# Kernel optimization log

Measured on AMD Instinct MI355X. Metric: run time of the kernel, lower is better.

## Reference

```python
import jax, jax.numpy as jnp
import numpy as np

B, S, C, T = 16, 64, 20, 2048
_DIMS = [(20, 20), (20, 20), (20, 20), (20, 10), (10, 1)]


def setup_inputs() -> dict:
    key = jax.random.key(0)
    keys = jax.random.split(key, 1 + 2 * len(_DIMS))
    inp = {"data": jax.random.normal(keys[0], (B, S, C, T), dtype=jnp.float32)}
    for i, (din, dout) in enumerate(_DIMS):
        # weights stored (in, out); scaled like torch's default Linear init
        inp[f"W{i+1}"] = jax.random.normal(keys[1 + 2 * i], (din, dout), dtype=jnp.float32) / jnp.sqrt(jnp.float32(din))
        inp[f"b{i+1}"] = jax.random.normal(keys[2 + 2 * i], (dout,), dtype=jnp.float32) * 0.05
    return inp


def _mlp(x, Ws, bs):
    # x: (..., in_dim); five Linear+ReLU layers, final ReLU included
    h = x
    for W, b in zip(Ws, bs):
        h = jax.nn.relu(h @ W + b)
    return h


def reference(data, W1, b1, W2, b2, W3, b3, W4, b4, W5, b5):
    # data: (B, S, C, T) -> per-time-point features (B, S, T, C)
    x = jnp.swapaxes(data, 2, 3)
    y = _mlp(x, (W1, W2, W3, W4, W5), (b1, b2, b3, b4, b5))[..., 0]  # (B, S, T)
    t = y.shape[-1]
    yc = y - y.mean(axis=-1, keepdims=True)
    cov = jnp.einsum('bst,but->bsu', yc, yc) / jnp.float32(t - 1)  # (B, S, S)
    d = jnp.sqrt(jnp.diagonal(cov, axis1=1, axis2=2))  # (B, S)
    corr = cov / (d[:, :, None] * d[:, None, :])
    corr = jnp.clip(corr, -1.0, 1.0)  # torch.corrcoef clips real output
    return 1.0 - corr
```

## Files before the change

kernel.cpp:

```cpp
#include <hip/hip_runtime.h>

#define Bn 16
#define Sn 64
#define Cn 20
#define Tn 2048
#define TPB 256

template <int NJ>
__device__ __forceinline__ void layer2(const float (&in)[2][20], float (&out)[2][20],
                                       const float* __restrict__ WT,
                                       const float* __restrict__ bb) {
    #pragma unroll
    for (int j = 0; j < NJ; ++j) {
        float a0 = bb[j], a1 = bb[j];
        const float4* wr = (const float4*)(WT + j * 20);
        #pragma unroll
        for (int q = 0; q < 5; ++q) {
            const float4 w = wr[q];
            a0 = fmaf(in[0][4 * q + 0], w.x, a0);  a1 = fmaf(in[1][4 * q + 0], w.x, a1);
            a0 = fmaf(in[0][4 * q + 1], w.y, a0);  a1 = fmaf(in[1][4 * q + 1], w.y, a1);
            a0 = fmaf(in[0][4 * q + 2], w.z, a0);  a1 = fmaf(in[1][4 * q + 2], w.z, a1);
            a0 = fmaf(in[0][4 * q + 3], w.w, a0);  a1 = fmaf(in[1][4 * q + 3], w.w, a1);
        }
        out[0][j] = fmaxf(a0, 0.f);
        out[1][j] = fmaxf(a1, 0.f);
    }
}

__global__ __launch_bounds__(256) void mlp_kernel(
    const float* __restrict__ data,
    const float* __restrict__ W1, const float* __restrict__ b1,
    const float* __restrict__ W2, const float* __restrict__ b2,
    const float* __restrict__ W3, const float* __restrict__ b3,
    const float* __restrict__ W4, const float* __restrict__ b4,
    const float* __restrict__ W5, const float* __restrict__ b5,
    float* __restrict__ y, double* __restrict__ Rp)
{
    __shared__ __align__(16) float sW1T[400], sW2T[400], sW3T[400], sW4T[200];
    __shared__ float sW5[10], sb1[20], sb2[20], sb3[20], sb4[10], sb5v[1];
    __shared__ double rbuf[TPB];

    const int tid = threadIdx.x;
    for (int i = tid; i < 400; i += TPB) {
        const int j = i / 20, c = i % 20;
        sW1T[i] = W1[c * 20 + j];
        sW2T[i] = W2[c * 20 + j];
        sW3T[i] = W3[c * 20 + j];
    }
    if (tid < 200) { const int j = tid / 20, c = tid % 20; sW4T[tid] = W4[c * 10 + j]; }
    if (tid < 20) { sb1[tid] = b1[tid]; sb2[tid] = b2[tid]; sb3[tid] = b3[tid]; }
    if (tid < 10) { sW5[tid] = W5[tid]; sb4[tid] = b4[tid]; }
    if (tid == 0) sb5v[0] = b5[0];
    __syncthreads();

    const int bs = blockIdx.x >> 2;
    const int qt = blockIdx.x & 3;
    const float* base = data + (size_t)bs * Cn * Tn;
    const int t0 = qt * (Tn / 4) + tid * 2;

    float x[2][20], h[2][20];
    #pragma unroll
    for (int c = 0; c < 20; ++c) {
        const float2 v = *(const float2*)&base[c * Tn + t0];
        x[0][c] = v.x; x[1][c] = v.y;
    }

    layer2<20>(x, h, sW1T, sb1);
    layer2<20>(h, x, sW2T, sb2);
    layer2<20>(x, h, sW3T, sb3);
    layer2<10>(h, x, sW4T, sb4);

    float yv[2];
    #pragma unroll
    for (int m = 0; m < 2; ++m) {
        float yy = sb5v[0];
        #pragma unroll
        for (int i = 0; i < 10; ++i) yy = fmaf(x[m][i], sW5[i], yy);
        yv[m] = fmaxf(yy, 0.f);
    }
    float2 st; st.x = yv[0]; st.y = yv[1];
    *(float2*)&y[(size_t)bs * Tn + t0] = st;

    rbuf[tid] = (double)yv[0] + (double)yv[1];
    __syncthreads();
    for (int off = 128; off > 0; off >>= 1) {
        if (tid < off) rbuf[tid] += rbuf[tid + off];
        __syncthreads();
    }
    if (tid == 0) Rp[blockIdx.x] = rbuf[0];
}

__global__ __launch_bounds__(256) void cov_kernel(
    const float* __restrict__ y, const double* __restrict__ Rp,
    double* __restrict__ covd)
{
    __shared__ __align__(16) float ysc[Tn];
    __shared__ double rbuf[TPB];

    const int tid = threadIdx.x;
    const int lane = tid & 63, wv = tid >> 6;
    const int ut = blockIdx.x & 3;
    const int bs = blockIdx.x >> 2;
    const int b = bs >> 6;

    const double ms = (Rp[bs * 4] + Rp[bs * 4 + 1] + Rp[bs * 4 + 2] + Rp[bs * 4 + 3]) * (1.0 / Tn);
    const float* yrow = y + (size_t)bs * Tn;

    double lsum = 0.0;
    for (int t = tid; t < Tn; t += TPB) {
        const float v = (float)((double)yrow[t] - ms);
        ysc[t] = v;
        lsum += (double)v;
    }
    rbuf[tid] = lsum;
    __syncthreads();
    for (int off = 128; off > 0; off >>= 1) {
        if (tid < off) rbuf[tid] += rbuf[tid + off];
        __syncthreads();
    }
    const double sumYsc = rbuf[0];

    const float* ybase = y + (size_t)(b << 6) * Tn;
    const double* Rb = Rp + (b << 6) * 4;
    double* crow = covd + (size_t)bs * Sn;

    #pragma unroll
    for (int uu = 0; uu < 4; ++uu) {
        const int u = ut * 16 + wv * 4 + uu;
        const float* yu = ybase + (size_t)u * Tn;
        float acc = 0.f;
        #pragma unroll
        for (int k = 0; k < Tn / 256; ++k) {
            const int t = (k * 64 + lane) * 4;
            const float4 a = *(const float4*)&ysc[t];
            const float4 g = *(const float4*)&yu[t];
            acc = fmaf(a.x, g.x, acc);
            acc = fmaf(a.y, g.y, acc);
            acc = fmaf(a.z, g.z, acc);
            acc = fmaf(a.w, g.w, acc);
        }
        #pragma unroll
        for (int off = 32; off; off >>= 1) acc += __shfl_down(acc, off, 64);
        if (lane == 0) {
            const double mu = (Rb[u * 4] + Rb[u * 4 + 1] + Rb[u * 4 + 2] + Rb[u * 4 + 3]) * (1.0 / Tn);
            crow[u] = ((double)acc - mu * sumYsc) * (1.0 / (Tn - 1));
        }
    }
}

__global__ __launch_bounds__(256) void corr_kernel(
    const double* __restrict__ covd, float* __restrict__ out)
{
    const int i = blockIdx.x * TPB + threadIdx.x;
    if (i >= Bn * Sn * Sn) return;
    const int b = i / (Sn * Sn);
    const int rem = i % (Sn * Sn);
    const int s = rem / Sn, u = rem % Sn;
    const double css = covd[((size_t)b * Sn + s) * Sn + s];
    const double cuu = covd[((size_t)b * Sn + u) * Sn + u];
    const double csu = covd[i];
    double r = csu / sqrt(css * cuu);
    r = (r < -1.0) ? -1.0 : ((r > 1.0) ? 1.0 : r);
    out[i] = (float)(1.0 - r);
}

extern "C" void kernel_launch(void* const* d_in, const int* in_sizes, int n_in,
                              void* d_out, int out_size, void* d_ws, size_t ws_size,
                              hipStream_t stream) {
    const float* data = (const float*)d_in[0];
    const float* W1 = (const float*)d_in[1];  const float* b1 = (const float*)d_in[2];
    const float* W2 = (const float*)d_in[3];  const float* b2 = (const float*)d_in[4];
    const float* W3 = (const float*)d_in[5];  const float* b3 = (const float*)d_in[6];
    const float* W4 = (const float*)d_in[7];  const float* b4 = (const float*)d_in[8];
    const float* W5 = (const float*)d_in[9];  const float* b5 = (const float*)d_in[10];
    float* out = (float*)d_out;

    float* y = (float*)d_ws;
    double* covd = (double*)((char*)d_ws + (size_t)Bn * Sn * Tn * sizeof(float));
    double* Rp = covd + (size_t)Bn * Sn * Sn;

    mlp_kernel<<<Bn * Sn * 4, TPB, 0, stream>>>(data, W1, b1, W2, b2, W3, b3, W4, b4, W5, b5, y, Rp);
    cov_kernel<<<Bn * Sn * 4, TPB, 0, stream>>>(y, Rp, covd);
    corr_kernel<<<(Bn * Sn * Sn + TPB - 1) / TPB, TPB, 0, stream>>>(covd, out);
}
```

Measured before the change: 316.2 us.

## Rewrite covariance as split-K register-tiled SYRK in shared memory with atomics

```diff
diff --git a/kernel.cpp b/kernel.cpp
--- a/kernel.cpp
+++ b/kernel.cpp
@@ -5,6 +5,9 @@
 #define Cn 20
 #define Tn 2048
 #define TPB 256
+#define KS 8
+#define Kc (Tn / KS)
+#define PITCH 260
 
 template <int NJ>
 __device__ __forceinline__ void layer2(const float (&in)[2][20], float (&out)[2][20],
@@ -92,73 +95,83 @@
 
 __global__ __launch_bounds__(256) void cov_kernel(
     const float* __restrict__ y, const double* __restrict__ Rp,
-    double* __restrict__ covd)
+    float* __restrict__ covf)
 {
-    __shared__ __align__(16) float ysc[Tn];
-    __shared__ double rbuf[TPB];
+    __shared__ __align__(16) float S[64 * PITCH];
+    __shared__ double smean[64];
 
     const int tid = threadIdx.x;
-    const int lane = tid & 63, wv = tid >> 6;
-    const int ut = blockIdx.x & 3;
-    const int bs = blockIdx.x >> 2;
-    const int b = bs >> 6;
+    const int b  = blockIdx.x >> 3;
+    const int ks = blockIdx.x & 7;
 
-    const double ms = (Rp[bs * 4] + Rp[bs * 4 + 1] + Rp[bs * 4 + 2] + Rp[bs * 4 + 3]) * (1.0 / Tn);
-    const float* yrow = y + (size_t)bs * Tn;
+    if (tid < 64) {
+        const int q = ((b << 6) + tid) * 4;
+        smean[tid] = (Rp[q] + Rp[q + 1] + Rp[q + 2] + Rp[q + 3]) * (1.0 / Tn);
+    }
+    __syncthreads();
 
-    double lsum = 0.0;
-    for (int t = tid; t < Tn; t += TPB) {
-        const float v = (float)((double)yrow[t] - ms);
-        ysc[t] = v;
-        lsum += (double)v;
+    const float* ybase = y + (size_t)(b << 6) * Tn + ks * Kc;
+    #pragma unroll
+    for (int it = 0; it < (64 * Kc / 4) / TPB; ++it) {
+        const int f4 = tid + it * TPB;
+        const int row = f4 >> 6;
+        const int k4 = f4 & 63;
+        const float4 v = *(const float4*)&ybase[(size_t)row * Tn + k4 * 4];
+        const double m = smean[row];
+        float4 c;
+        c.x = (float)((double)v.x - m);
+        c.y = (float)((double)v.y - m);
+        c.z = (float)((double)v.z - m);
+        c.w = (float)((double)v.w - m);
+        *(float4*)&S[row * PITCH + k4 * 4] = c;
     }
-    rbuf[tid] = lsum;
     __syncthreads();
-    for (int off = 128; off > 0; off >>= 1) {
-        if (tid < off) rbuf[tid] += rbuf[tid + off];
-        __syncthreads();
+
+    const int ty = tid >> 4, tx = tid & 15;
+    float acc[4][4];
+    #pragma unroll
+    for (int a = 0; a < 4; ++a)
+        #pragma unroll
+        for (int j = 0; j < 4; ++j) acc[a][j] = 0.f;
+
+    for (int kq = 0; kq < Kc / 4; ++kq) {
+        float4 av[4], bv[4];
+        #pragma unroll
+        for (int a = 0; a < 4; ++a) av[a] = *(const float4*)&S[(ty + 16 * a) * PITCH + kq * 4];
+        #pragma unroll
+        for (int j = 0; j < 4; ++j) bv[j] = *(const float4*)&S[(tx + 16 * j) * PITCH + kq * 4];
+        #pragma unroll
+        for (int a = 0; a < 4; ++a)
+            #pragma unroll
+            for (int j = 0; j < 4; ++j) {
+                acc[a][j] = fmaf(av[a].x, bv[j].x, acc[a][j]);
+                acc[a][j] = fmaf(av[a].y, bv[j].y, acc[a][j]);
+                acc[a][j] = fmaf(av[a].z, bv[j].z, acc[a][j]);
+                acc[a][j] = fmaf(av[a].w, bv[j].w, acc[a][j]);
+            }
     }
-    const double sumYsc = rbuf[0];
 
-    const float* ybase = y + (size_t)(b << 6) * Tn;
-    const double* Rb = Rp + (b << 6) * 4;
-    double* crow = covd + (size_t)bs * Sn;
-
+    float* cb = covf + ((size_t)b << 12);
     #pragma unroll
-    for (int uu = 0; uu < 4; ++uu) {
-        const int u = ut * 16 + wv * 4 + uu;
-        const float* yu = ybase + (size_t)u * Tn;
-        float acc = 0.f;
+    for (int a = 0; a < 4; ++a) {
+        const int row = ty + 16 * a;
         #pragma unroll
-        for (int k = 0; k < Tn / 256; ++k) {
-            const int t = (k * 64 + lane) * 4;
-            const float4 a = *(const float4*)&ysc[t];
-            const float4 g = *(const float4*)&yu[t];
-            acc = fmaf(a.x, g.x, acc);
-            acc = fmaf(a.y, g.y, acc);
-            acc = fmaf(a.z, g.z, acc);
-            acc = fmaf(a.w, g.w, acc);
-        }
-        #pragma unroll
-        for (int off = 32; off; off >>= 1) acc += __shfl_down(acc, off, 64);
-        if (lane == 0) {
-            const double mu = (Rb[u * 4] + Rb[u * 4 + 1] + Rb[u * 4 + 2] + Rb[u * 4 + 3]) * (1.0 / Tn);
-            crow[u] = ((double)acc - mu * sumYsc) * (1.0 / (Tn - 1));
-        }
+        for (int j = 0; j < 4; ++j)
+            atomicAdd(&cb[(row << 6) + tx + 16 * j], acc[a][j]);
     }
 }
 
 __global__ __launch_bounds__(256) void corr_kernel(
-    const double* __restrict__ covd, float* __restrict__ out)
+    const float* __restrict__ covf, float* __restrict__ out)
 {
     const int i = blockIdx.x * TPB + threadIdx.x;
     if (i >= Bn * Sn * Sn) return;
     const int b = i / (Sn * Sn);
     const int rem = i % (Sn * Sn);
     const int s = rem / Sn, u = rem % Sn;
-    const double css = covd[((size_t)b * Sn + s) * Sn + s];
-    const double cuu = covd[((size_t)b * Sn + u) * Sn + u];
-    const double csu = covd[i];
+    const double css = (double)covf[((size_t)b * Sn + s) * Sn + s];
+    const double cuu = (double)covf[((size_t)b * Sn + u) * Sn + u];
+    const double csu = (double)covf[i];
     double r = csu / sqrt(css * cuu);
     r = (r < -1.0) ? -1.0 : ((r > 1.0) ? 1.0 : r);
     out[i] = (float)(1.0 - r);
@@ -176,10 +189,11 @@
     float* out = (float*)d_out;
 
     float* y = (float*)d_ws;
-    double* covd = (double*)((char*)d_ws + (size_t)Bn * Sn * Tn * sizeof(float));
-    double* Rp = covd + (size_t)Bn * Sn * Sn;
+    float* covf = (float*)((char*)d_ws + (size_t)Bn * Sn * Tn * sizeof(float));
+    double* Rp = (double*)((char*)covf + (size_t)Bn * Sn * Sn * sizeof(float));
 
+    hipMemsetAsync(covf, 0, (size_t)Bn * Sn * Sn * sizeof(float), stream);
     mlp_kernel<<<Bn * Sn * 4, TPB, 0, stream>>>(data, W1, b1, W2, b2, W3, b3, W4, b4, W5, b5, y, Rp);
-    cov_kernel<<<Bn * Sn * 4, TPB, 0, stream>>>(y, Rp, covd);
-    corr_kernel<<<(Bn * Sn * Sn + TPB - 1) / TPB, TPB, 0, stream>>>(covd, out);
+    cov_kernel<<<Bn * KS, TPB, 0, stream>>>(y, Rp, covf);
+    corr_kernel<<<(Bn * Sn * Sn + TPB - 1) / TPB, TPB, 0, stream>>>(covf, out);
 }
```

Result: faster. 302.8 us (-4.2%).
